# Performance work log

Measured on AMD Instinct MI355X. Metric: run time of the kernel, lower is better.

The kernel has to match this reference:

```python
import jax, jax.numpy as jnp
import numpy as np

TEMP = 0.2
EPS = 1e-12


def _l2norm(v, axis=1):
    n = jnp.linalg.norm(v, axis=axis, keepdims=True)
    return v / jnp.maximum(n, EPS)


def setup_inputs() -> dict:
    key = jax.random.key(0)
    ks = jax.random.split(key, 7)
    B, D, P, K = 2048, 256, 100, 30
    return {
        "x": jax.random.normal(ks[0], (B, D), jnp.float32),
        "x_aug": jax.random.normal(ks[1], (B, D), jnp.float32),
        "proto_w": jax.random.normal(ks[2], (P, D), jnp.float32),
        "hard_q1": jax.random.randint(ks[3], (B,), 0, P, jnp.int32),
        "hard_q2": jax.random.randint(ks[4], (B,), 0, P, jnp.int32),
        "neg_q1": jax.random.randint(ks[5], (B, K), 0, P, jnp.int32),
        "neg_q2": jax.random.randint(ks[6], (B, K), 0, P, jnp.int32),
    }


def reference(x, x_aug, proto_w, hard_q1, hard_q2, neg_q1, neg_q2):
    B = x.shape[0]
    N = 2 * B
    P = proto_w.shape[0]

    out1 = _l2norm(x)                          # [B, D]
    out2 = _l2norm(x_aug)                      # [B, D]
    out = jnp.concatenate([out1, out2], axis=0)  # [N, D]
    hard_q = jnp.concatenate([hard_q1, hard_q2], axis=0)  # [N]
    neg_q = jnp.concatenate([neg_q1, neg_q2], axis=0)     # [N, K]

    sim = jnp.exp(jnp.matmul(out, out.T) / TEMP)  # [N, N]
    eye = jnp.eye(N, dtype=bool)

    # hard_selection: mask[i,j] = (i != j) and (hard_q[j] in neg_q[i])
    # build per-row prototype membership table [N, P] to avoid a [N, K, N] blowup
    member = jnp.zeros((N, P), dtype=bool).at[jnp.arange(N)[:, None], neg_q].set(True)
    mask = (~eye) & member[:, hard_q]  # member[i, hard_q[j]] -> [N, N]

    # sample_reweighting
    w = _l2norm(proto_w)                # normalized prototypes [P, D]
    proto_dist = jnp.matmul(w, w.T)     # cosine similarity [P, P]
    R = proto_dist[hard_q[:, None], hard_q[None, :]]  # [N, N]
    R = jnp.where(eye, 0.0, R)          # diag is 0 when the row min is taken
    rmin = jnp.min(R, axis=1, keepdims=True)
    R = jnp.where(eye, rmin, R)         # reweight[i][i] = min(reweight[i])
    rmax = jnp.max(R, axis=1, keepdims=True)
    R = (R - rmin) / (rmax - rmin)      # per-row min-max normalize
    mu = jnp.mean(R, axis=1, keepdims=True)
    std = jnp.std(R, axis=1, ddof=1, keepdims=True)  # torch.std is unbiased
    reweight = jnp.exp((R - mu) ** 2 / (2.0 * std ** 2))
    sim = sim * reweight

    # masked_select(...).sum() == global sum over masked entries (scalar)
    total = jnp.sum(jnp.where(mask, sim, 0.0))

    pos = jnp.exp(jnp.sum(out1 * out2, axis=-1) / TEMP)  # [B]
    pos = jnp.concatenate([pos, pos], axis=0)            # [N]
    loss = jnp.mean(-jnp.log(pos / total))
    return loss
```

## Files before the change

### kernel.cpp

```cpp
#include <hip/hip_runtime.h>
#include <hip/hip_bf16.h>
#include <cstdint>

#define B_ 2048
#define N_ 4096
#define D_ 256
#define P_ 100
#define K_ 30
#define INVT 5.0f
#define NTILE 64
#define NJOBS (NTILE * (NTILE + 1) / 2)
#define NBLK (NJOBS / 4)
#define NGRP 64

typedef __attribute__((ext_vector_type(8))) short bf16x8;
typedef __attribute__((ext_vector_type(4))) float f32x4;
typedef __attribute__((ext_vector_type(4))) unsigned short us4;

__device__ __forceinline__ float waveReduceSum(float v) {
#pragma unroll
  for (int off = 32; off > 0; off >>= 1) v += __shfl_xor(v, off, 64);
  return v;
}

__device__ __forceinline__ unsigned short f2bf(float f) {
  __hip_bfloat16 h = __float2bfloat16(f);
  return *reinterpret_cast<unsigned short*>(&h);
}
__device__ __forceinline__ float bf2f(unsigned short u) {
  return __uint_as_float(((unsigned int)u) << 16);
}

struct Ctrl {
  float sums[2];
  int ticket1;
  int pad;
  float partial[NGRP];
  int ticket0[NGRP];
};

__global__ __launch_bounds__(256) void prep_kernel(
    const float* __restrict__ x, const float* __restrict__ xa, const float* __restrict__ pw,
    const int* __restrict__ hq1, const int* __restrict__ hq2, int* __restrict__ hq,
    int* __restrict__ cnt, float* __restrict__ pd, __hip_bfloat16* __restrict__ outb,
    Ctrl* __restrict__ ctrl) {
  __shared__ int c[P_];
  __shared__ float s4[4];
  int t = threadIdx.x, lane = t & 63, wv = t >> 6;
  int bx = blockIdx.x;
  if (bx == 0) {
    if (t < 2) ctrl->sums[t] = 0.f;
    if (t == 2) ctrl->ticket1 = 0;
    if (t < NGRP) { ctrl->partial[t] = 0.f; ctrl->ticket0[t] = 0; }
    if (t < P_) c[t] = 0;
    __syncthreads();
    for (int i = t; i < N_; i += 256) {
      int q = (i < B_) ? hq1[i] : hq2[i - B_];
      hq[i] = q;
      atomicAdd(&c[q], 1);
    }
    __syncthreads();
    if (t < P_) cnt[t] = c[t];
  } else if (bx <= P_) {
    int q = bx - 1;
    float4 aq = ((const float4*)(pw + q * D_))[lane];
    float ssq = waveReduceSum(aq.x * aq.x + aq.y * aq.y + aq.z * aq.z + aq.w * aq.w);
    float qinv = 1.f / fmaxf(sqrtf(ssq), 1e-12f);
    for (int r = wv; r < P_; r += 4) {
      float4 b = ((const float4*)(pw + r * D_))[lane];
      float s = aq.x * b.x + aq.y * b.y + aq.z * b.z + aq.w * b.w;
      float n = b.x * b.x + b.y * b.y + b.z * b.z + b.w * b.w;
      s = waveReduceSum(s);
      n = waveReduceSum(n);
      if (lane == 0) pd[q * P_ + r] = s * qinv / fmaxf(sqrtf(n), 1e-12f);
    }
  } else {
    int i = (bx - 101) * 4 + wv;
    float4 a = ((const float4*)(x + i * D_))[lane];
    float ss = waveReduceSum(a.x * a.x + a.y * a.y + a.z * a.z + a.w * a.w);
    float inv1 = 1.f / fmaxf(sqrtf(ss), 1e-12f);
    float o1x = a.x * inv1, o1y = a.y * inv1, o1z = a.z * inv1, o1w = a.w * inv1;
    us4 p1; p1[0] = f2bf(o1x); p1[1] = f2bf(o1y); p1[2] = f2bf(o1z); p1[3] = f2bf(o1w);
    ((us4*)(outb + i * D_))[lane] = p1;
    float4 b = ((const float4*)(xa + i * D_))[lane];
    float ss2 = waveReduceSum(b.x * b.x + b.y * b.y + b.z * b.z + b.w * b.w);
    float inv2 = 1.f / fmaxf(sqrtf(ss2), 1e-12f);
    float o2x = b.x * inv2, o2y = b.y * inv2, o2z = b.z * inv2, o2w = b.w * inv2;
    us4 p2; p2[0] = f2bf(o2x); p2[1] = f2bf(o2y); p2[2] = f2bf(o2z); p2[3] = f2bf(o2w);
    ((us4*)(outb + (B_ + i) * D_))[lane] = p2;
    float d = waveReduceSum(o1x * o2x + o1y * o2y + o1z * o2z + o1w * o2w);
    if (lane == 0) s4[wv] = d;
    __syncthreads();
    if (t == 0) atomicAdd(&ctrl->sums[1], s4[0] + s4[1] + s4[2] + s4[3]);
  }
}

__global__ void gtab_kernel(const int* __restrict__ hq, const int* __restrict__ cnt,
                            const float* __restrict__ pd, const int* __restrict__ nq1,
                            const int* __restrict__ nq2, unsigned short* __restrict__ gtabh) {
  __shared__ unsigned char memb[4][104];
  int wv = threadIdx.x >> 6, lane = threadIdx.x & 63;
  int i = blockIdx.x * 4 + wv;
  int q = hq[i];
  if (lane < 52) { memb[wv][lane * 2] = 0; memb[wv][lane * 2 + 1] = 0; }
  __syncthreads();
  const int* nrow = (i < B_) ? (nq1 + i * K_) : (nq2 + (i - B_) * K_);
  if (lane < K_) memb[wv][nrow[lane]] = 1;
  __syncthreads();

  int p0 = lane, p1 = lane + 64;
  bool has1 = (p1 < P_);
  float v0 = pd[q * P_ + p0];
  int m0 = cnt[p0] - (p0 == q ? 1 : 0);
  float v1 = 0.f; int m1 = 0;
  if (has1) { v1 = pd[q * P_ + p1]; m1 = cnt[p1] - (p1 == q ? 1 : 0); }

  float mn = 1e30f, mx = -1e30f;
  if (m0 > 0) { mn = fminf(mn, v0); mx = fmaxf(mx, v0); }
  if (has1 && m1 > 0) { mn = fminf(mn, v1); mx = fmaxf(mx, v1); }
#pragma unroll
  for (int off = 32; off > 0; off >>= 1) {
    mn = fminf(mn, __shfl_xor(mn, off, 64));
    mx = fmaxf(mx, __shfl_xor(mx, off, 64));
  }
  float rmin = fminf(0.f, mn);
  float rmax = fmaxf(rmin, mx);
  float inv = 1.f / (rmax - rmin);
  float r0 = (v0 - rmin) * inv, r1 = (v1 - rmin) * inv;
  float s1 = (m0 > 0 ? (float)m0 * r0 : 0.f) + ((has1 && m1 > 0) ? (float)m1 * r1 : 0.f);
  s1 = waveReduceSum(s1);
  float mu = s1 / (float)N_;
  float ss = (m0 > 0 ? (float)m0 * (r0 - mu) * (r0 - mu) : 0.f) +
             ((has1 && m1 > 0) ? (float)m1 * (r1 - mu) * (r1 - mu) : 0.f);
  ss = waveReduceSum(ss);
  ss += mu * mu;
  float var = ss / (float)(N_ - 1);
  float i2v = 1.f / (2.f * var);
  float g0 = memb[wv][p0] ? __expf((r0 - mu) * (r0 - mu) * i2v) : 0.f;
  gtabh[i * P_ + p0] = f2bf(g0);
  if (has1) {
    float g1 = memb[wv][p1] ? __expf((r1 - mu) * (r1 - mu) * i2v) : 0.f;
    gtabh[i * P_ + p1] = f2bf(g1);
  }
}

__global__ __launch_bounds__(256) void tot_kernel(
    const __hip_bfloat16* __restrict__ outb, const unsigned short* __restrict__ gtabh,
    const int* __restrict__ hq, Ctrl* __restrict__ ctrl, float* __restrict__ out) {
  __shared__ float s4[4];
  const int tid = threadIdx.x, lane = tid & 63, wid = tid >> 6;
  const int r16 = lane & 15, k8 = lane >> 4;

  int rem = blockIdx.x * 4 + wid, ti = 0;
  while (rem >= NTILE - ti) { rem -= NTILE - ti; ++ti; }
  const int tj = ti + rem;
  const bool diag = (ti == tj);
  const int i0 = ti * 64, j0 = tj * 64;

  const __hip_bfloat16* Ab = outb + (i0 + r16) * D_ + k8 * 8;
  const __hip_bfloat16* Bb = outb + (j0 + r16) * D_ + k8 * 8;

  f32x4 acc[4][4] = {};
  bf16x8 a[2][4], b[2][4];
#pragma unroll
  for (int m = 0; m < 4; ++m) {
    a[0][m] = *(const bf16x8*)(Ab + m * 16 * D_);
    b[0][m] = *(const bf16x8*)(Bb + m * 16 * D_);
  }
#pragma unroll
  for (int kk = 0; kk < 8; ++kk) {
    const int cur = kk & 1, nxt = cur ^ 1;
    if (kk < 7) {
#pragma unroll
      for (int m = 0; m < 4; ++m) {
        a[nxt][m] = *(const bf16x8*)(Ab + m * 16 * D_ + (kk + 1) * 32);
        b[nxt][m] = *(const bf16x8*)(Bb + m * 16 * D_ + (kk + 1) * 32);
      }
    }
#pragma unroll
    for (int m = 0; m < 4; ++m)
#pragma unroll
      for (int n = 0; n < 4; ++n)
        acc[m][n] = __builtin_amdgcn_mfma_f32_16x16x32_bf16(a[cur][m], b[cur][n], acc[m][n], 0, 0, 0);
  }

  int4 hi4[4];
#pragma unroll
  for (int m = 0; m < 4; ++m) hi4[m] = *(const int4*)(hq + i0 + m * 16 + k8 * 4);
  int hj[4];
#pragma unroll
  for (int n = 0; n < 4; ++n) hj[n] = hq[j0 + n * 16 + r16];

  float local = 0.f;
  if (diag) {
#pragma unroll
    for (int m = 0; m < 4; ++m) {
#pragma unroll
      for (int n = 0; n < 4; ++n) {
#pragma unroll
        for (int r = 0; r < 4; ++r) {
          int il = m * 16 + k8 * 4 + r;
          int jl = n * 16 + r16;
          float e = __expf(acc[m][n][r] * INVT);
          float wv = bf2f(gtabh[(i0 + il) * P_ + hj[n]]);
          if (il != jl) local += wv * e;
        }
      }
    }
  } else {
#pragma unroll
    for (int m = 0; m < 4; ++m) {
#pragma unroll
      for (int n = 0; n < 4; ++n) {
#pragma unroll
        for (int r = 0; r < 4; ++r) {
          int i = i0 + m * 16 + k8 * 4 + r;
          int j = j0 + n * 16 + r16;
          float e = __expf(acc[m][n][r] * INVT);
          float wv = bf2f(gtabh[i * P_ + hj[n]]);
          int hi = ((const int*)&hi4[m])[r];
          wv += bf2f(gtabh[j * P_ + hi]);
          local += wv * e;
        }
      }
    }
  }
  local = waveReduceSum(local);
  if (lane == 0) s4[wid] = local;
  __syncthreads();
  if (tid == 0) {
    float blk = s4[0] + s4[1] + s4[2] + s4[3];
    const int g = blockIdx.x & (NGRP - 1);
    float old0 = atomicAdd(&ctrl->partial[g], blk);
    asm volatile("" ::"v"(old0));
    int cntg = (NBLK / NGRP) + (g < (NBLK & (NGRP - 1)) ? 1 : 0);
    int done0 = atomicAdd(&ctrl->ticket0[g], 1);
    if (done0 == cntg - 1) {
      float pg = atomicAdd(&ctrl->partial[g], 0.f);
      float old1 = atomicAdd(&ctrl->sums[0], pg);
      asm volatile("" ::"v"(old1));
      int done1 = atomicAdd(&ctrl->ticket1, 1);
      if (done1 == NGRP - 1) {
        float tot = atomicAdd(&ctrl->sums[0], 0.f);
        float pos = atomicAdd(&ctrl->sums[1], 0.f);
        out[0] = logf(tot) - pos * (INVT / (float)B_);
      }
    }
  }
}

extern "C" void kernel_launch(void* const* d_in, const int* in_sizes, int n_in,
                              void* d_out, int out_size, void* d_ws, size_t ws_size,
                              hipStream_t stream) {
  const float* x   = (const float*)d_in[0];
  const float* xa  = (const float*)d_in[1];
  const float* pw  = (const float*)d_in[2];
  const int* hq1   = (const int*)d_in[3];
  const int* hq2   = (const int*)d_in[4];
  const int* nq1   = (const int*)d_in[5];
  const int* nq2   = (const int*)d_in[6];
  float* out = (float*)d_out;

  char* ws = (char*)d_ws;
  __hip_bfloat16* outb  = (__hip_bfloat16*)(ws);
  unsigned short* gtabh = (unsigned short*)(ws + 2097152);
  float* pd    = (float*)(ws + 2916352);
  int*   hq    = (int*)  (ws + 2956800);
  int*   cnt   = (int*)  (ws + 2973184);
  Ctrl*  ctrl  = (Ctrl*) (ws + 2973696);

  prep_kernel<<<613, 256, 0, stream>>>(x, xa, pw, hq1, hq2, hq, cnt, pd, outb, ctrl);
  gtab_kernel<<<N_ / 4, 256, 0, stream>>>(hq, cnt, pd, nq1, nq2, gtabh);
  tot_kernel<<<NBLK, 256, 0, stream>>>(outb, gtabh, hq, ctrl, out);
}
```

Measured before the change: 131.7 us.

## Compute full NxN grid with 128x128 tiles and LDS-staged weight table

Replaces the triangular 64x64 tile schedule, which used symmetry and needed two weight-table lookups per element, with a full 32x32 grid of 128x128 tiles on 512-thread blocks. Each block stages its 128 rows of the weight table transposed in shared memory, so each element needs one vectorized LDS read instead of scattered global gathers. The cost is twice the MFMA and exp work, since symmetric tiles are no longer shared. Control-block resets and the positive-pair sum move into gtab_kernel through a per-block partial array instead of atomics.

Measured after the change: 139.4 us. +5.8%, slower.

```diff
diff --git a/kernel.cpp b/kernel.cpp
--- a/kernel.cpp
+++ b/kernel.cpp
@@ -8,9 +8,7 @@
 #define P_ 100
 #define K_ 30
 #define INVT 5.0f
-#define NTILE 64
-#define NJOBS (NTILE * (NTILE + 1) / 2)
-#define NBLK (NJOBS / 4)
+#define NBLK 1024
 #define NGRP 64
 
 typedef __attribute__((ext_vector_type(8))) short bf16x8;
@@ -43,15 +41,12 @@
     const float* __restrict__ x, const float* __restrict__ xa, const float* __restrict__ pw,
     const int* __restrict__ hq1, const int* __restrict__ hq2, int* __restrict__ hq,
     int* __restrict__ cnt, float* __restrict__ pd, __hip_bfloat16* __restrict__ outb,
-    Ctrl* __restrict__ ctrl) {
+    float* __restrict__ posarr) {
   __shared__ int c[P_];
   __shared__ float s4[4];
   int t = threadIdx.x, lane = t & 63, wv = t >> 6;
   int bx = blockIdx.x;
   if (bx == 0) {
-    if (t < 2) ctrl->sums[t] = 0.f;
-    if (t == 2) ctrl->ticket1 = 0;
-    if (t < NGRP) { ctrl->partial[t] = 0.f; ctrl->ticket0[t] = 0; }
     if (t < P_) c[t] = 0;
     __syncthreads();
     for (int i = t; i < N_; i += 256) {
@@ -91,13 +86,14 @@
     float d = waveReduceSum(o1x * o2x + o1y * o2y + o1z * o2z + o1w * o2w);
     if (lane == 0) s4[wv] = d;
     __syncthreads();
-    if (t == 0) atomicAdd(&ctrl->sums[1], s4[0] + s4[1] + s4[2] + s4[3]);
+    if (t == 0) posarr[bx - 101] = s4[0] + s4[1] + s4[2] + s4[3];
   }
 }
 
 __global__ void gtab_kernel(const int* __restrict__ hq, const int* __restrict__ cnt,
                             const float* __restrict__ pd, const int* __restrict__ nq1,
-                            const int* __restrict__ nq2, unsigned short* __restrict__ gtabh) {
+                            const int* __restrict__ nq2, unsigned short* __restrict__ gtabh,
+                            const float* __restrict__ posarr, Ctrl* __restrict__ ctrl) {
   __shared__ unsigned char memb[4][104];
   int wv = threadIdx.x >> 6, lane = threadIdx.x & 63;
   int i = blockIdx.x * 4 + wv;
@@ -142,100 +138,116 @@
     float g1 = memb[wv][p1] ? __expf((r1 - mu) * (r1 - mu) * i2v) : 0.f;
     gtabh[i * P_ + p1] = f2bf(g1);
   }
-}
-
-__global__ __launch_bounds__(256) void tot_kernel(
+
+  if (blockIdx.x == 0) {
+    int t = threadIdx.x;
+    if (t >= 64 && t < 128) { ctrl->partial[t - 64] = 0.f; }
+    else if (t >= 128 && t < 192) { ctrl->ticket0[t - 128] = 0; }
+    else if (t == 192) { ctrl->ticket1 = 0; }
+    else if (t == 193) { ctrl->sums[0] = 0.f; }
+    if (t < 64) {
+      float s = 0.f;
+#pragma unroll
+      for (int e = 0; e < 8; ++e) s += posarr[t + e * 64];
+      s = waveReduceSum(s);
+      if (t == 0) ctrl->sums[1] = s;
+    }
+  }
+}
+
+__global__ __launch_bounds__(512) void tot_kernel(
     const __hip_bfloat16* __restrict__ outb, const unsigned short* __restrict__ gtabh,
     const int* __restrict__ hq, Ctrl* __restrict__ ctrl, float* __restrict__ out) {
-  __shared__ float s4[4];
+  __shared__ unsigned short gaT[P_ * 132];
+  __shared__ int hqj[128];
+  __shared__ float s8[8];
   const int tid = threadIdx.x, lane = tid & 63, wid = tid >> 6;
   const int r16 = lane & 15, k8 = lane >> 4;
-
-  int rem = blockIdx.x * 4 + wid, ti = 0;
-  while (rem >= NTILE - ti) { rem -= NTILE - ti; ++ti; }
-  const int tj = ti + rem;
-  const bool diag = (ti == tj);
-  const int i0 = ti * 64, j0 = tj * 64;
-
-  const __hip_bfloat16* Ab = outb + (i0 + r16) * D_ + k8 * 8;
-  const __hip_bfloat16* Bb = outb + (j0 + r16) * D_ + k8 * 8;
-
-  f32x4 acc[4][4] = {};
-  bf16x8 a[2][4], b[2][4];
-#pragma unroll
-  for (int m = 0; m < 4; ++m) {
-    a[0][m] = *(const bf16x8*)(Ab + m * 16 * D_);
-    b[0][m] = *(const bf16x8*)(Bb + m * 16 * D_);
-  }
+  const int bi = blockIdx.x >> 5, bj = blockIdx.x & 31;
+  const bool diag = (bi == bj);
+  const int i0 = bi * 128, j0 = bj * 128;
+  const int qr = wid >> 2, qc = wid & 3;
+  const int iw = i0 + qr * 64, jw = j0 + qc * 32;
+
+  for (int idx = tid; idx < 128 * P_; idx += 512) {
+    int r = idx / P_, c = idx - r * P_;
+    gaT[c * 132 + r] = gtabh[(i0 + r) * P_ + c];
+  }
+  if (tid < 128) hqj[tid] = hq[j0 + tid];
+
+  const __hip_bfloat16* Ab = outb + (iw + r16) * D_ + k8 * 8;
+  const __hip_bfloat16* Bb = outb + (jw + r16) * D_ + k8 * 8;
+
+  f32x4 acc[4][2] = {};
+  bf16x8 a[2][4], b[2][2];
+#pragma unroll
+  for (int m = 0; m < 4; ++m) a[0][m] = *(const bf16x8*)(Ab + m * 16 * D_);
+#pragma unroll
+  for (int n = 0; n < 2; ++n) b[0][n] = *(const bf16x8*)(Bb + n * 16 * D_);
 #pragma unroll
   for (int kk = 0; kk < 8; ++kk) {
     const int cur = kk & 1, nxt = cur ^ 1;
     if (kk < 7) {
 #pragma unroll
-      for (int m = 0; m < 4; ++m) {
-        a[nxt][m] = *(const bf16x8*)(Ab + m * 16 * D_ + (kk + 1) * 32);
-        b[nxt][m] = *(const bf16x8*)(Bb + m * 16 * D_ + (kk + 1) * 32);
-      }
+      for (int m = 0; m < 4; ++m) a[nxt][m] = *(const bf16x8*)(Ab + m * 16 * D_ + (kk + 1) * 32);
+#pragma unroll
+      for (int n = 0; n < 2; ++n) b[nxt][n] = *(const bf16x8*)(Bb + n * 16 * D_ + (kk + 1) * 32);
     }
 #pragma unroll
     for (int m = 0; m < 4; ++m)
 #pragma unroll
-      for (int n = 0; n < 4; ++n)
+      for (int n = 0; n < 2; ++n)
         acc[m][n] = __builtin_amdgcn_mfma_f32_16x16x32_bf16(a[cur][m], b[cur][n], acc[m][n], 0, 0, 0);
   }
-
-  int4 hi4[4];
-#pragma unroll
-  for (int m = 0; m < 4; ++m) hi4[m] = *(const int4*)(hq + i0 + m * 16 + k8 * 4);
-  int hj[4];
-#pragma unroll
-  for (int n = 0; n < 4; ++n) hj[n] = hq[j0 + n * 16 + r16];
+  __syncthreads();
+
+  int hj[2];
+#pragma unroll
+  for (int n = 0; n < 2; ++n) hj[n] = hqj[qc * 32 + n * 16 + r16];
 
   float local = 0.f;
   if (diag) {
 #pragma unroll
     for (int m = 0; m < 4; ++m) {
-#pragma unroll
-      for (int n = 0; n < 4; ++n) {
+      int ilb = qr * 64 + m * 16 + k8 * 4;
+#pragma unroll
+      for (int n = 0; n < 2; ++n) {
+        us4 w = *(const us4*)(gaT + hj[n] * 132 + ilb);
+        int jl = qc * 32 + n * 16 + r16;
 #pragma unroll
         for (int r = 0; r < 4; ++r) {
-          int il = m * 16 + k8 * 4 + r;
-          int jl = n * 16 + r16;
           float e = __expf(acc[m][n][r] * INVT);
-          float wv = bf2f(gtabh[(i0 + il) * P_ + hj[n]]);
-          if (il != jl) local += wv * e;
+          if (ilb + r != jl) local += bf2f(w[r]) * e;
         }
       }
     }
   } else {
 #pragma unroll
     for (int m = 0; m < 4; ++m) {
-#pragma unroll
-      for (int n = 0; n < 4; ++n) {
+      int ilb = qr * 64 + m * 16 + k8 * 4;
+#pragma unroll
+      for (int n = 0; n < 2; ++n) {
+        us4 w = *(const us4*)(gaT + hj[n] * 132 + ilb);
 #pragma unroll
         for (int r = 0; r < 4; ++r) {
-          int i = i0 + m * 16 + k8 * 4 + r;
-          int j = j0 + n * 16 + r16;
           float e = __expf(acc[m][n][r] * INVT);
-          float wv = bf2f(gtabh[i * P_ + hj[n]]);
-          int hi = ((const int*)&hi4[m])[r];
-          wv += bf2f(gtabh[j * P_ + hi]);
-          local += wv * e;
+          local += bf2f(w[r]) * e;
         }
       }
     }
   }
   local = waveReduceSum(local);
-  if (lane == 0) s4[wid] = local;
+  if (lane == 0) s8[wid] = local;
   __syncthreads();
   if (tid == 0) {
-    float blk = s4[0] + s4[1] + s4[2] + s4[3];
+    float blk = 0.f;
+#pragma unroll
+    for (int w = 0; w < 8; ++w) blk += s8[w];
     const int g = blockIdx.x & (NGRP - 1);
     float old0 = atomicAdd(&ctrl->partial[g], blk);
     asm volatile("" ::"v"(old0));
-    int cntg = (NBLK / NGRP) + (g < (NBLK & (NGRP - 1)) ? 1 : 0);
     int done0 = atomicAdd(&ctrl->ticket0[g], 1);
-    if (done0 == cntg - 1) {
+    if (done0 == (NBLK / NGRP) - 1) {
       float pg = atomicAdd(&ctrl->partial[g], 0.f);
       float old1 = atomicAdd(&ctrl->sums[0], pg);
       asm volatile("" ::"v"(old1));
@@ -268,8 +280,9 @@
   int*   hq    = (int*)  (ws + 2956800);
   int*   cnt   = (int*)  (ws + 2973184);
   Ctrl*  ctrl  = (Ctrl*) (ws + 2973696);
-
-  prep_kernel<<<613, 256, 0, stream>>>(x, xa, pw, hq1, hq2, hq, cnt, pd, outb, ctrl);
-  gtab_kernel<<<N_ / 4, 256, 0, stream>>>(hq, cnt, pd, nq1, nq2, gtabh);
-  tot_kernel<<<NBLK, 256, 0, stream>>>(outb, gtabh, hq, ctrl, out);
-}
+  float* posarr= (float*)(ws + 2974336);
+
+  prep_kernel<<<613, 256, 0, stream>>>(x, xa, pw, hq1, hq2, hq, cnt, pd, outb, posarr);
+  gtab_kernel<<<N_ / 4, 256, 0, stream>>>(hq, cnt, pd, nq1, nq2, gtabh, posarr, ctrl);
+  tot_kernel<<<NBLK, 512, 0, stream>>>(outb, gtabh, hq, ctrl, out);
+}
```
